# Kernel tuning notes

Measured on AMD Instinct MI355X. Metric: run time of the kernel, lower is better.

The kernel has to match this reference:

```python
import jax, jax.numpy as jnp
import numpy as np

# Mamba3TextEncoder config (class .small() defaults)
B_SZ, SEQ = 4, 512
VOCAB, D_MODEL, N_LAYERS = 32000, 768, 12
N_STATE, EXPAND, HEADDIM, NGROUPS, EMBED = 64, 2, 32, 1, 1536
D_INNER = EXPAND * D_MODEL            # 1536
NHEADS = D_INNER // HEADDIM           # 48
CONV_DIM = D_INNER + 2 * NGROUPS * N_STATE  # 1664 (x, B, C go through depthwise conv)
K_CONV = 4
PROJ_IN = 2 * D_INNER + 2 * NGROUPS * N_STATE + NHEADS  # z, xBC, dt


def setup_inputs() -> dict:
    key = jax.random.key(0)
    ks = jax.random.split(key, 16)
    s = 0.02
    return {
        "token_ids": jax.random.randint(ks[0], (B_SZ, SEQ), 0, VOCAB),
        "embed_W": jax.random.normal(ks[1], (VOCAB, D_MODEL), jnp.float32) * s,
        "ln_W": jnp.ones((N_LAYERS, D_MODEL), jnp.float32),
        "in_proj_W": jax.random.normal(ks[2], (N_LAYERS, D_MODEL, PROJ_IN), jnp.float32) * s,
        "conv_W": jax.random.normal(ks[3], (N_LAYERS, CONV_DIM, 1, K_CONV), jnp.float32) * 0.1,
        "conv_b": jnp.zeros((N_LAYERS, CONV_DIM), jnp.float32),
        "dt_bias": jax.random.uniform(ks[4], (N_LAYERS, NHEADS), jnp.float32, -4.6, -2.0),
        "A_log": jnp.tile(jnp.log(jnp.arange(1, NHEADS + 1, dtype=jnp.float32))[None], (N_LAYERS, 1)),
        "D": jnp.ones((N_LAYERS, NHEADS), jnp.float32),
        "norm_W": jnp.ones((N_LAYERS, D_INNER), jnp.float32),
        "out_proj_W": jax.random.normal(ks[5], (N_LAYERS, D_INNER, D_MODEL), jnp.float32) * s,
        "final_norm_W": jnp.ones((D_MODEL,), jnp.float32),
        "proj_W": jax.random.normal(ks[6], (D_MODEL, EMBED), jnp.float32) * s,
        "proj_b": jnp.zeros((EMBED,), jnp.float32),
    }


def _rmsnorm(x, w, eps=1e-5):
    return x * jax.lax.rsqrt(jnp.mean(x * x, axis=-1, keepdims=True) + eps) * w


def _causal_conv(x, w, b):
    # x: [B,S,C] depthwise causal conv, kernel K_CONV
    y = jax.lax.conv_general_dilated(
        x.transpose(0, 2, 1), w, (1,), [(K_CONV - 1, 0)],
        dimension_numbers=("NCH", "OIH", "NCH"), feature_group_count=CONV_DIM)
    return y.transpose(0, 2, 1) + b


def _ssm(xs, dt, A, Bm, Cm):
    # selective scan. xs:[B,S,H,P] dt:[B,S,H] A:[H] Bm,Cm:[B,S,N] (ngroups=1)
    decay = jnp.exp(dt * A)              # [B,S,H]
    dtx = dt[..., None] * xs             # [B,S,H,P]
    h0 = jnp.zeros((xs.shape[0], NHEADS, HEADDIM, N_STATE), xs.dtype)

    def step(h, inp):
        dec, dx, b, c = inp              # [B,H],[B,H,P],[B,N],[B,N]
        h = dec[..., None, None] * h + dx[..., None] * b[:, None, None, :]
        y = jnp.einsum("bhpn,bn->bhp", h, c)
        return h, y

    inputs = (decay.transpose(1, 0, 2), dtx.transpose(1, 0, 2, 3),
              Bm.transpose(1, 0, 2), Cm.transpose(1, 0, 2))
    _, ys = jax.lax.scan(step, h0, inputs)
    return ys.transpose(1, 0, 2, 3)      # [B,S,H,P]


def reference(token_ids, embed_W, ln_W, in_proj_W, conv_W, conv_b, dt_bias,
              A_log, D, norm_W, out_proj_W, final_norm_W, proj_W, proj_b):
    x = embed_W[token_ids]                               # [B,S,D]
    for l in range(N_LAYERS):
        h = _rmsnorm(x, ln_W[l])
        zxbcdt = h @ in_proj_W[l]                        # [B,S,PROJ_IN]
        z = zxbcdt[..., :D_INNER]
        xBC = zxbcdt[..., D_INNER:D_INNER + CONV_DIM]
        dt_raw = zxbcdt[..., D_INNER + CONV_DIM:]        # [B,S,H]
        xBC = jax.nn.silu(_causal_conv(xBC, conv_W[l], conv_b[l]))
        xs = xBC[..., :D_INNER].reshape(*xBC.shape[:2], NHEADS, HEADDIM)
        Bm = xBC[..., D_INNER:D_INNER + N_STATE]
        Cm = xBC[..., D_INNER + N_STATE:]
        dt = jax.nn.softplus(dt_raw + dt_bias[l])
        A = -jnp.exp(A_log[l])
        y = _ssm(xs, dt, A, Bm, Cm) + D[l][None, None, :, None] * xs
        y = y.reshape(*y.shape[:2], D_INNER)
        y = _rmsnorm(y * jax.nn.silu(z), norm_W[l])      # gated RMSNorm
        x = x + y @ out_proj_W[l]
    x = _rmsnorm(x, final_norm_W)
    pooled = x.mean(axis=1)                              # [B,D]
    proj = pooled @ proj_W + proj_b                      # [B,EMBED]
    n = jnp.sqrt(jnp.sum(proj * proj, axis=-1, keepdims=True))
    return proj / jnp.maximum(n, 1e-12)
```

## Files before the change

### kernel.cpp

```cpp
#include <hip/hip_runtime.h>
#include <math.h>

typedef __bf16 bf16x8 __attribute__((ext_vector_type(8)));
typedef short  s16x8  __attribute__((ext_vector_type(8)));
typedef float  f32x4  __attribute__((ext_vector_type(4)));

static constexpr int BSZ = 4, SEQ = 512, DM = 768;
static constexpr int DIN = 1536, NH = 48, HP = 32, NS = 64;
static constexpr int CDIM = 1664;
static constexpr int PROJ_IN = 3248;
static constexpr int LDZX = 3328;
static constexpr int ROWS = BSZ * SEQ;
static constexpr int EMBED = 1536;
static constexpr int NLAYERS = 12;

using gptr_t = const __attribute__((address_space(1))) void*;
using lptr_t = __attribute__((address_space(3))) void*;

__device__ __forceinline__ unsigned short f2bf(float f) {
  unsigned u = __builtin_bit_cast(unsigned, f);
  u += 0x7FFF + ((u >> 16) & 1);
  return (unsigned short)(u >> 16);
}
__device__ __forceinline__ float bf2f(unsigned short u) {
  unsigned v = (unsigned)u << 16;
  return __builtin_bit_cast(float, v);
}
__device__ __forceinline__ float sigm(float x) { return 1.f / (1.f + __expf(-x)); }
__device__ __forceinline__ float sp(float x) { return (x > 15.f) ? x : log1pf(__expf(x)); }

__device__ __forceinline__ void gll16(const void* g, void* l) {
  __builtin_amdgcn_global_load_lds((gptr_t)g, (lptr_t)l, 16, 0, 0);
}
__device__ __forceinline__ f32x4 mfma16(s16x8 a, s16x8 b, f32x4 c) {
  return __builtin_amdgcn_mfma_f32_16x16x32_bf16(
      __builtin_bit_cast(bf16x8, a), __builtin_bit_cast(bf16x8, b), c, 0, 0, 0);
}

template <int NW>
__device__ __forceinline__ float block_sum(float v) {
#pragma unroll
  for (int o = 32; o; o >>= 1) v += __shfl_xor(v, o);
  __shared__ float red[NW];
  if ((threadIdx.x & 63) == 0) red[threadIdx.x >> 6] = v;
  __syncthreads();
  float s = red[0];
#pragma unroll
  for (int i = 1; i < NW; ++i) s += red[i];
  return s;
}

__global__ void embed_k(const int* __restrict__ tok, const float* __restrict__ eW,
                        float* __restrict__ x, unsigned short* __restrict__ x16,
                        float* __restrict__ ssq1p) {
  int bt = blockIdx.x, tid = threadIdx.x;
  float4 v = ((const float4*)(eW + (size_t)tok[bt] * DM))[tid];
  ((float4*)(x + (size_t)bt * DM))[tid] = v;
  unsigned long long pk =
      (unsigned long long)f2bf(v.x) | ((unsigned long long)f2bf(v.y) << 16) |
      ((unsigned long long)f2bf(v.z) << 32) | ((unsigned long long)f2bf(v.w) << 48);
  *(unsigned long long*)(x16 + (size_t)bt * DM + tid * 4) = pk;
  float ss = v.x * v.x + v.y * v.y + v.z * v.z + v.w * v.w;
  float tot = block_sum<3>(ss);
  if (tid < 12) ssq1p[(size_t)bt * 12 + tid] = (tid == 0) ? tot : 0.f;
}

__global__ void transpose_cvt(const float* __restrict__ W, const float* __restrict__ sc,
                              unsigned short* __restrict__ Wt, int K, int N, int Npad) {
  __shared__ float tile[32][68];
  int l = blockIdx.z;
  const float* Wl = W + (size_t)l * K * N;
  const float* scl = sc + (size_t)l * K;
  unsigned short* Wtl = Wt + (size_t)l * Npad * K;
  int nb = blockIdx.x * 64, kb = blockIdx.y * 32;
  int tid = threadIdx.x;
#pragma unroll
  for (int rep = 0; rep < 2; ++rep) {
    int f = rep * 256 + tid;
    int k = f >> 4, c4 = f & 15;
    int n = nb + c4 * 4;
    float s = scl[kb + k];
    float4 v = {0.f, 0.f, 0.f, 0.f};
    if (n + 3 < N) {
      v = *(const float4*)(Wl + (size_t)(kb + k) * N + n);
    } else if (n < N) {
      float t_[4] = {0.f, 0.f, 0.f, 0.f};
      for (int j = 0; j < 4; ++j) if (n + j < N) t_[j] = Wl[(size_t)(kb + k) * N + n + j];
      v = {t_[0], t_[1], t_[2], t_[3]};
    }
    tile[k][c4 * 4 + 0] = v.x * s; tile[k][c4 * 4 + 1] = v.y * s;
    tile[k][c4 * 4 + 2] = v.z * s; tile[k][c4 * 4 + 3] = v.w * s;
  }
  __syncthreads();
#pragma unroll
  for (int rep = 0; rep < 2; ++rep) {
    int f = rep * 256 + tid;
    int n = f >> 3, k8 = f & 7;
    unsigned long long pk =
        (unsigned long long)f2bf(tile[k8 * 4 + 0][n]) |
        ((unsigned long long)f2bf(tile[k8 * 4 + 1][n]) << 16) |
        ((unsigned long long)f2bf(tile[k8 * 4 + 2][n]) << 32) |
        ((unsigned long long)f2bf(tile[k8 * 4 + 3][n]) << 48);
    *(unsigned long long*)(Wtl + (size_t)(nb + n) * K + kb + k8 * 4) = pk;
  }
}

template <int BM, int BN, int BK, int NWARP, int MODE>
__global__ __launch_bounds__(NWARP * 64) void gemm_k(
    const unsigned short* __restrict__ A, const unsigned short* __restrict__ Bt,
    int K, const float* __restrict__ ssqp, void* __restrict__ O0,
    void* __restrict__ O1, void* __restrict__ O2,
    unsigned short* __restrict__ x16o, float* __restrict__ ssqo) {
  constexpr int THR = NWARP * 64;
  constexpr int WROWS = BM / NWARP;
  constexpr int FM = WROWS / 16, FN = BN / 16, KS = BK / 32, CH = BK / 8;
  constexpr int AIT = (BM * CH) / THR, BIT = (BN * CH) / THR, NST = AIT + BIT;
  constexpr int NSSQ = (MODE == 0) ? 12 : 48;
  constexpr float INVD = (MODE == 0) ? (1.f / 768.f) : (1.f / 1536.f);
  __shared__ unsigned short lA[2][BM * BK], lB[2][BN * BK];
  __shared__ float rss[BM];
  int tid = threadIdx.x, lane = tid & 63, wv = tid >> 6;
  int flat = blockIdx.y * gridDim.x + blockIdx.x;
  int q8 = (gridDim.x * gridDim.y) >> 3;
  int nf = (flat & 7) * q8 + (flat >> 3);
  int bx = nf % gridDim.x, by = nf / gridDim.x;
  int m0 = by * BM, n0 = bx * BN;
  int wm = wv * WROWS;
  int NK = K / BK;
  auto stage = [&](int kt, int buf) {
#pragma unroll
    for (int i = 0; i < AIT; ++i) {
      int flt = i * THR + tid, rr = flt / CH, cc = flt % CH;
      gll16(A + (size_t)(m0 + rr) * K + kt + ((cc ^ (rr & 7)) * 8),
            (char*)lA[buf] + flt * 16);
    }
#pragma unroll
    for (int i = 0; i < BIT; ++i) {
      int flt = i * THR + tid, rr = flt / CH, cc = flt % CH;
      gll16(Bt + (size_t)(n0 + rr) * K + kt + ((cc ^ (rr & 7)) * 8),
            (char*)lB[buf] + flt * 16);
    }
  };
  stage(0, 0);
  if (tid < BM) {
    const float* p = ssqp + (size_t)(m0 + tid) * NSSQ;
    float s = 0.f;
#pragma unroll
    for (int j = 0; j < NSSQ; ++j) s += p[j];
    rss[tid] = rsqrtf(s * INVD + 1e-5f);
  }
  __syncthreads();
  f32x4 acc[FM][FN] = {};
  for (int i = 0; i < NK; ++i) {
    if (i + 1 < NK) {
      stage((i + 1) * BK, (i + 1) & 1);
      asm volatile("s_waitcnt vmcnt(%0)" :: "i"(NST) : "memory");
    } else {
      asm volatile("s_waitcnt vmcnt(0)" ::: "memory");
    }
    __builtin_amdgcn_s_barrier();
    __builtin_amdgcn_sched_barrier(0);
    const unsigned short* cA = lA[i & 1];
    const unsigned short* cB = lB[i & 1];
    __builtin_amdgcn_s_setprio(1);
#pragma unroll
    for (int ks = 0; ks < KS; ++ks) {
      s16x8 a[FM], b[FN];
#pragma unroll
      for (int mi = 0; mi < FM; ++mi) {
        int row = wm + mi * 16 + (lane & 15);
        int ch = (ks * 4 + (lane >> 4)) ^ (row & 7);
        a[mi] = *(const s16x8*)((const char*)cA + row * (CH * 16) + ch * 16);
      }
#pragma unroll
      for (int nj = 0; nj < FN; ++nj) {
        int row = nj * 16 + (lane & 15);
        int ch = (ks * 4 + (lane >> 4)) ^ (row & 7);
        b[nj] = *(const s16x8*)((const char*)cB + row * (CH * 16) + ch * 16);
      }
#pragma unroll
      for (int mi = 0; mi < FM; ++mi)
#pragma unroll
        for (int nj = 0; nj < FN; ++nj)
          acc[mi][nj] = mfma16(a[mi], b[nj], acc[mi][nj]);
    }
    __builtin_amdgcn_s_setprio(0);
    __builtin_amdgcn_s_barrier();
  }
#pragma unroll
  for (int mi = 0; mi < FM; ++mi) {
    int rl0 = wm + mi * 16 + ((lane >> 4) << 2);
    float rsr[4];
#pragma unroll
    for (int rg = 0; rg < 4; ++rg) rsr[rg] = rss[rl0 + rg];
    float part[4] = {0.f, 0.f, 0.f, 0.f};
#pragma unroll
    for (int nj = 0; nj < FN; ++nj) {
      int col = n0 + nj * 16 + (lane & 15);
#pragma unroll
      for (int rg = 0; rg < 4; ++rg) {
        int row = m0 + rl0 + rg;
        float vv = acc[mi][nj][rg] * rsr[rg];
        if constexpr (MODE == 0) {
          if (n0 < DIN) {
            ((unsigned short*)O0)[(size_t)row * DIN + col] = f2bf(vv);
          } else if (n0 < DIN + CDIM) {
            ((float*)O1)[(size_t)row * CDIM + (col - DIN)] = vv;
          } else {
            int c2 = col - (DIN + CDIM);
            if (c2 < NH) ((float*)O2)[(size_t)row * NH + c2] = vv;
          }
        } else {
          size_t idx = (size_t)row * DM + col;
          float xn = vv + ((float*)O0)[idx];
          ((float*)O0)[idx] = xn;
          x16o[idx] = f2bf(xn);
          part[rg] += xn * xn;
        }
      }
    }
    if constexpr (MODE == 1) {
#pragma unroll
      for (int rg = 0; rg < 4; ++rg) {
#pragma unroll
        for (int off = 1; off < 16; off <<= 1) part[rg] += __shfl_xor(part[rg], off);
      }
      if ((lane & 15) == 0) {
#pragma unroll
        for (int rg = 0; rg < 4; ++rg)
          ssqo[(size_t)(m0 + rl0 + rg) * 12 + bx] = part[rg];
      }
    }
  }
}

__global__ __launch_bounds__(256) void conv_dt_k(
    const float* __restrict__ xbc, const float* __restrict__ cw, const float* __restrict__ cb,
    const float* __restrict__ dtraw, const float* __restrict__ dbias,
    unsigned short* __restrict__ xs16, unsigned short* __restrict__ dtxT,
    unsigned short* __restrict__ Bbf, unsigned short* __restrict__ Cbf,
    float* __restrict__ dts) {
  __shared__ float stg[11][256];
  __shared__ float dtl[8][48];
  int tid = threadIdx.x;
  int chunk = blockIdx.x;
  int bt0 = blockIdx.y * 8;
  int t0 = bt0 & (SEQ - 1);
  int cbase = chunk * 256;
  for (int f = tid; f < 11 * 64; f += 256) {
    int row = f >> 6, c4 = f & 63;
    int s = t0 - 3 + row;
    int col = cbase + c4 * 4;
    float4 v = {0.f, 0.f, 0.f, 0.f};
    if (s >= 0 && col + 3 < CDIM) {
      v = *(const float4*)(xbc + (size_t)(bt0 - 3 + row) * CDIM + col);
    }
    *(float4*)&stg[row][c4 * 4] = v;
  }
  if (chunk < 6) {
    for (int idx = tid; idx < 384; idx += 256) {
      int r = idx / 48, hh = idx - r * 48;
      dtl[r][hh] = sp(dtraw[(size_t)(bt0 + r) * NH + hh] + dbias[hh]);
    }
  }
  __syncthreads();
  int c = cbase + tid;
  if (chunk < 6) {
    float w0 = cw[c * 4], w1 = cw[c * 4 + 1], w2 = cw[c * 4 + 2], w3 = cw[c * 4 + 3];
    float bias = cb[c];
    int hh = c >> 5, p = c & 31, b = bt0 >> 9;
    s16x8 pk;
#pragma unroll
    for (int r = 0; r < 8; ++r) {
      float a = bias + stg[r][tid] * w0 + stg[r + 1][tid] * w1 + stg[r + 2][tid] * w2 +
                stg[r + 3][tid] * w3;
      float sv = a * sigm(a);
      xs16[(size_t)(bt0 + r) * DIN + c] = f2bf(sv);
      pk[r] = (short)f2bf(sv * dtl[r][hh]);
    }
    *reinterpret_cast<s16x8*>(dtxT + ((((size_t)b * NH + hh) * HP + p) * SEQ + t0)) = pk;
  } else if (tid < 128) {
    int cc = DIN + tid;
    float w0 = cw[cc * 4], w1 = cw[cc * 4 + 1], w2 = cw[cc * 4 + 2], w3 = cw[cc * 4 + 3];
    float bias = cb[cc];
#pragma unroll
    for (int r = 0; r < 8; ++r) {
      float a = bias + stg[r][tid] * w0 + stg[r + 1][tid] * w1 + stg[r + 2][tid] * w2 +
                stg[r + 3][tid] * w3;
      float sv = a * sigm(a);
      if (tid < 64) Bbf[(size_t)(bt0 + r) * NS + tid] = f2bf(sv);
      else          Cbf[(size_t)(bt0 + r) * NS + (tid - 64)] = f2bf(sv);
    }
  } else if (tid < 176) {
    int hh = tid - 128;
    float bias_ = dbias[hh];
    float v[8];
#pragma unroll
    for (int r = 0; r < 8; ++r) v[r] = sp(dtraw[(size_t)(bt0 + r) * NH + hh] + bias_);
    float4 a4 = {v[0], v[1], v[2], v[3]}, b4 = {v[4], v[5], v[6], v[7]};
    float* dp = dts + ((size_t)(bt0 >> 9) * NH + hh) * SEQ + t0;
    *(float4*)dp = a4;
    *(float4*)(dp + 4) = b4;
  }
}

__global__ __launch_bounds__(256) void scan_k(
    const unsigned short* __restrict__ Bbf, const unsigned short* __restrict__ Cbf,
    const unsigned short* __restrict__ dtxT, const unsigned short* __restrict__ xs16,
    const float* __restrict__ dts, const unsigned short* __restrict__ zb,
    const float* __restrict__ alog, const float* __restrict__ Dvec,
    unsigned short* __restrict__ g16, float* __restrict__ ssq2p) {
  __shared__ unsigned short CbPt[64 * 64];
  __shared__ unsigned short Bb[2][64 * 64], Dx[2][32 * 64];
  __shared__ float lsb[SEQ];
  __shared__ float wtot[4];
  __shared__ int sfirst;
  int tid = threadIdx.x, lane = tid & 63, wv = tid >> 6;
  int tb = blockIdx.x, h = blockIdx.y, b = blockIdx.z;
  int t0 = tb * 64;
  const unsigned short* dxrow = dtxT + ((size_t)b * NH + h) * HP * SEQ;

#pragma unroll
  for (int i = 0; i < 2; ++i) {
    int flt = i * 256 + tid, rr = flt >> 3, cc = flt & 7;
    gll16(Cbf + (size_t)(b * SEQ + t0 + rr) * NS + (cc ^ (rr & 7)) * 8, (char*)CbPt + flt * 16);
  }
  float Ah = -__expf(alog[h]);
  int t2 = tid * 2;
  float2 dv = *(const float2*)(dts + ((size_t)b * NH + h) * SEQ + t2);
  float d0 = dv.x * Ah, d1 = dv.y * Ah;
  float ps = d0 + d1;
  float v = ps;
#pragma unroll
  for (int off = 1; off < 64; off <<= 1) {
    float u = __shfl_up(v, off);
    if (lane >= off) v += u;
  }
  if (lane == 63) wtot[wv] = v;
  if (tid == 0) sfirst = tb;
  __syncthreads();
  float wpre = 0.f;
#pragma unroll
  for (int w = 0; w < 3; ++w) wpre += (w < wv) ? wtot[w] : 0.f;
  float excl = v + wpre - ps;
  lsb[t2] = excl + d0;
  lsb[t2 + 1] = excl + d0 + d1;
  __syncthreads();
  float REF = lsb[t0];
  if (tid < tb && (REF - lsb[tid * 64 + 63] >= -12.f)) atomicMin(&sfirst, tid);
  __syncthreads();
  int st0 = sfirst;

#pragma unroll
  for (int i = 0; i < 2; ++i) {
    int flt = i * 256 + tid, rr = flt >> 3, cc = flt & 7;
    gll16(Bbf + (size_t)(b * SEQ + st0 * 64 + rr) * NS + (cc ^ (rr & 7)) * 8,
          (char*)Bb[st0 & 1] + flt * 16);
  }
  { int rr = tid >> 3, cc = tid & 7;
    gll16(dxrow + (size_t)rr * SEQ + st0 * 64 + (cc ^ (rr & 7)) * 8,
          (char*)Dx[st0 & 1] + tid * 16); }

  float lt[4], elt[4];
  int trb = wv * 16 + ((lane >> 4) << 2);
#pragma unroll
  for (int rg = 0; rg < 4; ++rg) {
    lt[rg] = lsb[t0 + trb + rg];
    elt[rg] = __expf(lt[rg] - REF);
  }
  s16x8 aC[2];
  f32x4 yacc[2] = {};

  for (int st = st0; st <= tb; ++st) {
    int s0 = st * 64;
    if (st < tb) {
      int s1 = s0 + 64;
#pragma unroll
      for (int i = 0; i < 2; ++i) {
        int flt = i * 256 + tid, rr = flt >> 3, cc = flt & 7;
        gll16(Bbf + (size_t)(b * SEQ + s1 + rr) * NS + (cc ^ (rr & 7)) * 8,
              (char*)Bb[(st + 1) & 1] + flt * 16);
      }
      { int rr = tid >> 3, cc = tid & 7;
        gll16(dxrow + (size_t)rr * SEQ + s1 + (cc ^ (rr & 7)) * 8,
              (char*)Dx[(st + 1) & 1] + tid * 16); }
      asm volatile("s_waitcnt vmcnt(3)" ::: "memory");
    } else {
      asm volatile("s_waitcnt vmcnt(0)" ::: "memory");
    }
    __builtin_amdgcn_s_barrier();
    __builtin_amdgcn_sched_barrier(0);
    const unsigned short* Bcur = Bb[st & 1];
    const unsigned short* Dcur = Dx[st & 1];
    if (st == st0) {
#pragma unroll
      for (int ks = 0; ks < 2; ++ks) {
        int row = wv * 16 + (lane & 15);
        int ch = (ks * 4 + (lane >> 4)) ^ (row & 7);
        aC[ks] = *(const s16x8*)((const char*)CbPt + row * 128 + ch * 16);
      }
    }
    float lsv[4];
#pragma unroll
    for (int sq = 0; sq < 4; ++sq) lsv[sq] = lsb[s0 + sq * 16 + (lane & 15)];
    f32x4 gf[4] = {};
    __builtin_amdgcn_s_setprio(1);
#pragma unroll
    for (int sq = 0; sq < 4; ++sq)
#pragma unroll
      for (int ks = 0; ks < 2; ++ks) {
        int row = sq * 16 + (lane & 15);
        int ch = (ks * 4 + (lane >> 4)) ^ (row & 7);
        s16x8 bB = *(const s16x8*)((const char*)Bcur + row * 128 + ch * 16);
        gf[sq] = mfma16(aC[ks], bB, gf[sq]);
      }
    __builtin_amdgcn_s_setprio(0);
    if (st < tb) {
      float es[4];
#pragma unroll
      for (int sq = 0; sq < 4; ++sq) es[sq] = __expf(REF - lsv[sq]);
#pragma unroll
      for (int sq = 0; sq < 4; ++sq) {
        int scol = sq * 16 + (lane & 15);
#pragma unroll
        for (int rg = 0; rg < 4; ++rg) {
          int trow = trb + rg;
          int off = (trow * 128 + scol * 2) ^ ((trow & 7) << 4);
          *(unsigned short*)((char*)CbPt + off) = f2bf(gf[sq][rg] * (elt[rg] * es[sq]));
        }
      }
    } else {
#pragma unroll
      for (int sq = 0; sq < 4; ++sq) {
        int scol = sq * 16 + (lane & 15);
        int sg = s0 + scol;
#pragma unroll
        for (int rg = 0; rg < 4; ++rg) {
          int trow = trb + rg, tg = t0 + trow;
          float wgt = (sg <= tg) ? __expf(lt[rg] - lsv[sq]) : 0.f;
          int off = (trow * 128 + scol * 2) ^ ((trow & 7) << 4);
          *(unsigned short*)((char*)CbPt + off) = f2bf(gf[sq][rg] * wgt);
        }
      }
    }
    __builtin_amdgcn_s_setprio(1);
#pragma unroll
    for (int ks = 0; ks < 2; ++ks) {
      int row = wv * 16 + (lane & 15);
      int ch = (ks * 4 + (lane >> 4)) ^ (row & 7);
      s16x8 aP = *(const s16x8*)((const char*)CbPt + row * 128 + ch * 16);
#pragma unroll
      for (int pq = 0; pq < 2; ++pq) {
        int prow = pq * 16 + (lane & 15);
        int pch = (ks * 4 + (lane >> 4)) ^ (prow & 7);
        s16x8 bD = *(const s16x8*)((const char*)Dcur + prow * 128 + pch * 16);
        yacc[pq] = mfma16(aP, bD, yacc[pq]);
      }
    }
    __builtin_amdgcn_s_setprio(0);
    __builtin_amdgcn_s_barrier();
  }
  float Dh = Dvec[h];
  float part[4] = {0.f, 0.f, 0.f, 0.f};
#pragma unroll
  for (int pq = 0; pq < 2; ++pq) {
#pragma unroll
    for (int rg = 0; rg < 4; ++rg) {
      int trow = trb + rg;
      int tg = t0 + trow;
      int p = pq * 16 + (lane & 15);
      size_t gi = (size_t)(b * SEQ + tg) * DIN + h * HP + p;
      float xv = bf2f(xs16[gi]);
      float yv = yacc[pq][rg] + Dh * xv;
      float zf = bf2f(zb[gi]);
      float g = yv * zf * sigm(zf);
      g16[gi] = f2bf(g);
      part[rg] += g * g;
    }
  }
#pragma unroll
  for (int rg = 0; rg < 4; ++rg) {
#pragma unroll
    for (int off = 1; off < 16; off <<= 1) part[rg] += __shfl_xor(part[rg], off);
  }
  if ((lane & 15) == 0) {
#pragma unroll
    for (int rg = 0; rg < 4; ++rg)
      ssq2p[(size_t)(b * SEQ + t0 + trb + rg) * 48 + h] = part[rg];
  }
}

__global__ void pool_k(const float* __restrict__ x, const float* __restrict__ ssq1p,
                       const float* __restrict__ fnW, float* __restrict__ pooled) {
  __shared__ float rsl[SEQ];
  int b = blockIdx.y, d0 = blockIdx.x * 256;
  for (int t = threadIdx.x; t < SEQ; t += 256) {
    const float* p = ssq1p + (size_t)(b * SEQ + t) * 12;
    float s = 0.f;
#pragma unroll
    for (int j = 0; j < 12; ++j) s += p[j];
    rsl[t] = rsqrtf(s * (1.f / DM) + 1e-5f);
  }
  __syncthreads();
  int d = d0 + threadIdx.x;
  float s = 0.f;
  for (int t = 0; t < SEQ; ++t) s += x[(size_t)(b * SEQ + t) * DM + d] * rsl[t];
  pooled[b * DM + d] = s * (1.f / SEQ) * fnW[d];
}
__global__ void proj_k(const float* __restrict__ pooled, const float* __restrict__ pW,
                       const float* __restrict__ pb, float* __restrict__ ptmp) {
  int e0 = blockIdx.x * 64, b = blockIdx.y;
  int el = threadIdx.x & 63, g = threadIdx.x >> 6;
  int e = e0 + el;
  float s = 0.f;
  for (int d = g * 192; d < (g + 1) * 192; ++d)
    s += pooled[b * DM + d] * pW[(size_t)d * EMBED + e];
  __shared__ float red[4][64];
  red[g][el] = s;
  __syncthreads();
  if (g == 0) ptmp[b * EMBED + e] = red[0][el] + red[1][el] + red[2][el] + red[3][el] + pb[e];
}
__global__ void l2_k(const float* __restrict__ ptmp, float* __restrict__ out) {
  int b = blockIdx.x;
  float v[6], ss = 0.f;
#pragma unroll
  for (int i = 0; i < 6; ++i) {
    v[i] = ptmp[(size_t)b * EMBED + threadIdx.x + i * 256];
    ss += v[i] * v[i];
  }
  float tot = block_sum<4>(ss);
  float inv = 1.f / fmaxf(sqrtf(tot), 1e-12f);
#pragma unroll
  for (int i = 0; i < 6; ++i)
    out[(size_t)b * EMBED + threadIdx.x + i * 256] = v[i] * inv;
}

extern "C" void kernel_launch(void* const* d_in, const int* in_sizes, int n_in,
                              void* d_out, int out_size, void* d_ws, size_t ws_size,
                              hipStream_t stream) {
  const int*   tok  = (const int*)d_in[0];
  const float* embW = (const float*)d_in[1];
  const float* lnW  = (const float*)d_in[2];
  const float* ipW  = (const float*)d_in[3];
  const float* cW   = (const float*)d_in[4];
  const float* cB   = (const float*)d_in[5];
  const float* dtB  = (const float*)d_in[6];
  const float* Alog = (const float*)d_in[7];
  const float* Dv   = (const float*)d_in[8];
  const float* nW   = (const float*)d_in[9];
  const float* opW  = (const float*)d_in[10];
  const float* fnW  = (const float*)d_in[11];
  const float* pW   = (const float*)d_in[12];
  const float* pb   = (const float*)d_in[13];
  float* out = (float*)d_out;

  char* wsp = (char*)d_ws;
  auto alloc = [&](size_t bytes) {
    char* p = wsp;
    wsp += (bytes + 255) & ~(size_t)255;
    return p;
  };
  float* x      = (float*)alloc((size_t)ROWS * DM * 4);
  float* xbc    = (float*)alloc((size_t)ROWS * CDIM * 4);
  float* dtraw  = (float*)alloc((size_t)ROWS * NH * 4);
  float* dts    = (float*)alloc((size_t)BSZ * NH * SEQ * 4);
  float* ssq1p  = (float*)alloc((size_t)ROWS * 12 * 4);
  float* ssq2p  = (float*)alloc((size_t)ROWS * 48 * 4);
  float* pooled = (float*)alloc((size_t)BSZ * DM * 4);
  float* ptmp   = (float*)alloc((size_t)BSZ * EMBED * 4);
  unsigned short* x16   = (unsigned short*)alloc((size_t)ROWS * DM * 2);
  unsigned short* zb    = (unsigned short*)alloc((size_t)ROWS * DIN * 2);
  unsigned short* xs16  = (unsigned short*)alloc((size_t)ROWS * DIN * 2);
  unsigned short* g16   = (unsigned short*)alloc((size_t)ROWS * DIN * 2);
  unsigned short* dtxT  = (unsigned short*)alloc((size_t)BSZ * NH * HP * SEQ * 2);
  unsigned short* Bbf   = (unsigned short*)alloc((size_t)ROWS * NS * 2);
  unsigned short* Cbf   = (unsigned short*)alloc((size_t)ROWS * NS * 2);
  unsigned short* wtA   = (unsigned short*)alloc((size_t)NLAYERS * LDZX * DM * 2);
  unsigned short* wtO   = (unsigned short*)alloc((size_t)NLAYERS * DM * DIN * 2);

  embed_k<<<ROWS, 192, 0, stream>>>(tok, embW, x, x16, ssq1p);
  transpose_cvt<<<dim3(LDZX / 64, DM / 32, NLAYERS), 256, 0, stream>>>(
      ipW, lnW, wtA, DM, PROJ_IN, LDZX);
  transpose_cvt<<<dim3(DM / 64, DIN / 32, NLAYERS), 256, 0, stream>>>(
      opW, nW, wtO, DIN, DM, DM);

  for (int l = 0; l < NLAYERS; ++l) {
    gemm_k<128, 128, 64, 2, 0><<<dim3(LDZX / 128, ROWS / 128), 128, 0, stream>>>(
        x16, wtA + (size_t)l * LDZX * DM, DM, ssq1p, zb, xbc, dtraw, nullptr, nullptr);
    conv_dt_k<<<dim3(7, ROWS / 8), 256, 0, stream>>>(
        xbc, cW + (size_t)l * CDIM * 4, cB + (size_t)l * CDIM, dtraw, dtB + l * NH,
        xs16, dtxT, Bbf, Cbf, dts);
    scan_k<<<dim3(SEQ / 64, NH, BSZ), 256, 0, stream>>>(
        Bbf, Cbf, dtxT, xs16, dts, zb, Alog + l * NH, Dv + l * NH, g16, ssq2p);
    gemm_k<64, 64, 128, 2, 1><<<dim3(DM / 64, ROWS / 64), 128, 0, stream>>>(
        g16, wtO + (size_t)l * DM * DIN, DIN, ssq2p, x, x, nullptr, x16, ssq1p);
  }

  pool_k<<<dim3(DM / 256, BSZ), 256, 0, stream>>>(x, ssq1p, fnW, pooled);
  proj_k<<<dim3(EMBED / 64, BSZ), 256, 0, stream>>>(pooled, pW, pb, ptmp);
  l2_k<<<BSZ, 256, 0, stream>>>(ptmp, out);
}
```

Measured before the change: 1.111 ms.

## Use 2x2 four-wave GEMM tiling with fixed BK=64 and split row-sum partials

```diff
diff --git a/kernel.cpp b/kernel.cpp
--- a/kernel.cpp
+++ b/kernel.cpp
@@ -62,7 +62,7 @@
   *(unsigned long long*)(x16 + (size_t)bt * DM + tid * 4) = pk;
   float ss = v.x * v.x + v.y * v.y + v.z * v.z + v.w * v.w;
   float tot = block_sum<3>(ss);
-  if (tid < 12) ssq1p[(size_t)bt * 12 + tid] = (tid == 0) ? tot : 0.f;
+  if (tid < 24) ssq1p[(size_t)bt * 24 + tid] = (tid == 0) ? tot : 0.f;
 }
 
 __global__ void transpose_cvt(const float* __restrict__ W, const float* __restrict__ sc,
@@ -105,19 +105,17 @@
   }
 }
 
-template <int BM, int BN, int BK, int NWARP, int MODE>
-__global__ __launch_bounds__(NWARP * 64) void gemm_k(
+template <int BM, int BN, int MODE>
+__global__ __launch_bounds__(256) void gemm_k(
     const unsigned short* __restrict__ A, const unsigned short* __restrict__ Bt,
     int K, const float* __restrict__ ssqp, void* __restrict__ O0,
     void* __restrict__ O1, void* __restrict__ O2,
     unsigned short* __restrict__ x16o, float* __restrict__ ssqo) {
-  constexpr int THR = NWARP * 64;
-  constexpr int WROWS = BM / NWARP;
-  constexpr int FM = WROWS / 16, FN = BN / 16, KS = BK / 32, CH = BK / 8;
-  constexpr int AIT = (BM * CH) / THR, BIT = (BN * CH) / THR, NST = AIT + BIT;
-  constexpr int NSSQ = (MODE == 0) ? 12 : 48;
+  constexpr int AIT = BM / 32, BIT = BN / 32, NST = AIT + BIT;
+  constexpr int FM = BM / 32, FN = BN / 32;
+  constexpr int NSSQ = (MODE == 0) ? 24 : 48;
   constexpr float INVD = (MODE == 0) ? (1.f / 768.f) : (1.f / 1536.f);
-  __shared__ unsigned short lA[2][BM * BK], lB[2][BN * BK];
+  __shared__ unsigned short lA[2][BM * 64], lB[2][BN * 64];
   __shared__ float rss[BM];
   int tid = threadIdx.x, lane = tid & 63, wv = tid >> 6;
   int flat = blockIdx.y * gridDim.x + blockIdx.x;
@@ -125,20 +123,18 @@
   int nf = (flat & 7) * q8 + (flat >> 3);
   int bx = nf % gridDim.x, by = nf / gridDim.x;
   int m0 = by * BM, n0 = bx * BN;
-  int wm = wv * WROWS;
-  int NK = K / BK;
+  int wm = (wv >> 1) * (BM / 2), wn = (wv & 1) * (BN / 2);
+  int NK = K >> 6;
   auto stage = [&](int kt, int buf) {
 #pragma unroll
     for (int i = 0; i < AIT; ++i) {
-      int flt = i * THR + tid, rr = flt / CH, cc = flt % CH;
-      gll16(A + (size_t)(m0 + rr) * K + kt + ((cc ^ (rr & 7)) * 8),
-            (char*)lA[buf] + flt * 16);
+      int flt = i * 256 + tid, rr = flt >> 3, cc = flt & 7;
+      gll16(A + (size_t)(m0 + rr) * K + kt + (cc ^ (rr & 7)) * 8, (char*)lA[buf] + flt * 16);
     }
 #pragma unroll
     for (int i = 0; i < BIT; ++i) {
-      int flt = i * THR + tid, rr = flt / CH, cc = flt % CH;
-      gll16(Bt + (size_t)(n0 + rr) * K + kt + ((cc ^ (rr & 7)) * 8),
-            (char*)lB[buf] + flt * 16);
+      int flt = i * 256 + tid, rr = flt >> 3, cc = flt & 7;
+      gll16(Bt + (size_t)(n0 + rr) * K + kt + (cc ^ (rr & 7)) * 8, (char*)lB[buf] + flt * 16);
     }
   };
   stage(0, 0);
@@ -153,7 +149,7 @@
   f32x4 acc[FM][FN] = {};
   for (int i = 0; i < NK; ++i) {
     if (i + 1 < NK) {
-      stage((i + 1) * BK, (i + 1) & 1);
+      stage((i + 1) << 6, (i + 1) & 1);
       asm volatile("s_waitcnt vmcnt(%0)" :: "i"(NST) : "memory");
     } else {
       asm volatile("s_waitcnt vmcnt(0)" ::: "memory");
@@ -162,21 +158,20 @@
     __builtin_amdgcn_sched_barrier(0);
     const unsigned short* cA = lA[i & 1];
     const unsigned short* cB = lB[i & 1];
-    __builtin_amdgcn_s_setprio(1);
-#pragma unroll
-    for (int ks = 0; ks < KS; ++ks) {
+#pragma unroll
+    for (int ks = 0; ks < 2; ++ks) {
       s16x8 a[FM], b[FN];
 #pragma unroll
       for (int mi = 0; mi < FM; ++mi) {
         int row = wm + mi * 16 + (lane & 15);
         int ch = (ks * 4 + (lane >> 4)) ^ (row & 7);
-        a[mi] = *(const s16x8*)((const char*)cA + row * (CH * 16) + ch * 16);
+        a[mi] = *(const s16x8*)((const char*)cA + row * 128 + ch * 16);
       }
 #pragma unroll
       for (int nj = 0; nj < FN; ++nj) {
-        int row = nj * 16 + (lane & 15);
+        int row = wn + nj * 16 + (lane & 15);
         int ch = (ks * 4 + (lane >> 4)) ^ (row & 7);
-        b[nj] = *(const s16x8*)((const char*)cB + row * (CH * 16) + ch * 16);
+        b[nj] = *(const s16x8*)((const char*)cB + row * 128 + ch * 16);
       }
 #pragma unroll
       for (int mi = 0; mi < FM; ++mi)
@@ -184,7 +179,6 @@
         for (int nj = 0; nj < FN; ++nj)
           acc[mi][nj] = mfma16(a[mi], b[nj], acc[mi][nj]);
     }
-    __builtin_amdgcn_s_setprio(0);
     __builtin_amdgcn_s_barrier();
   }
 #pragma unroll
@@ -196,7 +190,7 @@
     float part[4] = {0.f, 0.f, 0.f, 0.f};
 #pragma unroll
     for (int nj = 0; nj < FN; ++nj) {
-      int col = n0 + nj * 16 + (lane & 15);
+      int col = n0 + wn + nj * 16 + (lane & 15);
 #pragma unroll
       for (int rg = 0; rg < 4; ++rg) {
         int row = m0 + rl0 + rg;
@@ -228,7 +222,7 @@
       if ((lane & 15) == 0) {
 #pragma unroll
         for (int rg = 0; rg < 4; ++rg)
-          ssqo[(size_t)(m0 + rl0 + rg) * 12 + bx] = part[rg];
+          ssqo[(size_t)(m0 + rl0 + rg) * 24 + bx * 2 + (wn >> 5)] = part[rg];
       }
     }
   }
@@ -495,10 +489,10 @@
   __shared__ float rsl[SEQ];
   int b = blockIdx.y, d0 = blockIdx.x * 256;
   for (int t = threadIdx.x; t < SEQ; t += 256) {
-    const float* p = ssq1p + (size_t)(b * SEQ + t) * 12;
+    const float* p = ssq1p + (size_t)(b * SEQ + t) * 24;
     float s = 0.f;
 #pragma unroll
-    for (int j = 0; j < 12; ++j) s += p[j];
+    for (int j = 0; j < 24; ++j) s += p[j];
     rsl[t] = rsqrtf(s * (1.f / DM) + 1e-5f);
   }
   __syncthreads();
@@ -564,7 +558,7 @@
   float* xbc    = (float*)alloc((size_t)ROWS * CDIM * 4);
   float* dtraw  = (float*)alloc((size_t)ROWS * NH * 4);
   float* dts    = (float*)alloc((size_t)BSZ * NH * SEQ * 4);
-  float* ssq1p  = (float*)alloc((size_t)ROWS * 12 * 4);
+  float* ssq1p  = (float*)alloc((size_t)ROWS * 24 * 4);
   float* ssq2p  = (float*)alloc((size_t)ROWS * 48 * 4);
   float* pooled = (float*)alloc((size_t)BSZ * DM * 4);
   float* ptmp   = (float*)alloc((size_t)BSZ * EMBED * 4);
@@ -585,15 +579,15 @@
       opW, nW, wtO, DIN, DM, DM);
 
   for (int l = 0; l < NLAYERS; ++l) {
-    gemm_k<128, 128, 64, 2, 0><<<dim3(LDZX / 128, ROWS / 128), 128, 0, stream>>>(
+    gemm_k<128, 128, 0><<<dim3(LDZX / 128, ROWS / 128), 256, 0, stream>>>(
         x16, wtA + (size_t)l * LDZX * DM, DM, ssq1p, zb, xbc, dtraw, nullptr, nullptr);
     conv_dt_k<<<dim3(7, ROWS / 8), 256, 0, stream>>>(
         xbc, cW + (size_t)l * CDIM * 4, cB + (size_t)l * CDIM, dtraw, dtB + l * NH,
         xs16, dtxT, Bbf, Cbf, dts);
     scan_k<<<dim3(SEQ / 64, NH, BSZ), 256, 0, stream>>>(
         Bbf, Cbf, dtxT, xs16, dts, zb, Alog + l * NH, Dv + l * NH, g16, ssq2p);
-    gemm_k<64, 64, 128, 2, 1><<<dim3(DM / 64, ROWS / 64), 128, 0, stream>>>(
-        g16, wtO + (size_t)l * DM * DIN, DIN, ssq2p, x, x, nullptr, x16, ssq1p);
+    gemm_k<64, 64, 1><<<dim3(DM / 64, ROWS / 64), 256, 0, stream>>>(
+        g16, wtO + (size_t)l * DM * DIN, DIN, ssq2p, x, nullptr, nullptr, x16, ssq1p);
   }
 
   pool_k<<<dim3(DM / 256, BSZ), 256, 0, stream>>>(x, ssq1p, fnW, pooled);
```

Result: faster. 937.8 us (-15.6%).
